# Performance work log

Measured on AMD Instinct MI355X. Metric: run time of the kernel, lower is better.

## Reference

```python
import jax, jax.numpy as jnp
import numpy as np

B, N, H, D = 16, 512, 8, 128  # batch, nodes, heads, hid_dim (per-head dim == hid_dim)


def setup_inputs() -> dict:
    key = jax.random.key(0)
    ks = jax.random.split(key, 12)
    x = jax.random.normal(ks[0], (B, N, D), dtype=jnp.float32)
    dist = jax.random.normal(ks[1], (B, N, N), dtype=jnp.float32)
    mask = (jax.random.uniform(ks[2], (B, N)) < 0.9).astype(jnp.float32)
    w_std = 0.02
    Wq = jax.random.normal(ks[3], (D, H * D), dtype=jnp.float32) * w_std
    Wk = jax.random.normal(ks[4], (D, H * D), dtype=jnp.float32) * w_std
    Wv = jax.random.normal(ks[5], (D, H * D), dtype=jnp.float32) * w_std
    Wo = jax.random.normal(ks[6], (H * D, D), dtype=jnp.float32) * w_std
    bq = jax.random.normal(ks[7], (H * D,), dtype=jnp.float32) * w_std
    bk = jax.random.normal(ks[8], (H * D,), dtype=jnp.float32) * w_std
    bv = jax.random.normal(ks[9], (H * D,), dtype=jnp.float32) * w_std
    bo = jax.random.normal(ks[10], (D,), dtype=jnp.float32) * w_std
    return {"x": x, "dist": dist, "mask": mask,
            "Wq": Wq, "bq": bq, "Wk": Wk, "bk": bk,
            "Wv": Wv, "bv": bv, "Wo": Wo, "bo": bo}


def reference(x, dist, mask, Wq, bq, Wk, bk, Wv, bv, Wo, bo):
    scale = jnp.asarray(D, x.dtype) ** -0.5
    # projections: [B,N,H*D] -> [B,H,N,D]
    q = (x @ Wq + bq).reshape(B, N, H, D).transpose(0, 2, 1, 3)
    k = (x @ Wk + bk).reshape(B, N, H, D).transpose(0, 2, 1, 3)
    v = (x @ Wv + bv).reshape(B, N, H, D).transpose(0, 2, 1, 3)
    m = mask[:, None, :, None]  # [B,1,N,1]
    q = q * m * scale
    k = k * m
    v = v * m
    a = jnp.einsum('bhnd,bhmd->bhnm', q, k)  # [B,H,N,N]
    a = a + dist[:, None, :, :]  # dist bias broadcast over heads
    amask = (mask[:, :, None] * mask[:, None, :])[:, None, :, :]  # [B,1,N,N]
    a = jnp.where(amask == 0, jnp.asarray(-1e9, a.dtype), a)
    a = jax.nn.softmax(a, axis=-1)
    a = jnp.where(amask == 0, jnp.asarray(0.0, a.dtype), a)
    y = jnp.einsum('bhnm,bhmd->bhnd', a, v)
    y = y.transpose(0, 2, 1, 3).reshape(B, N, H * D)
    y = y @ Wo + bo
    return y * mask[:, :, None]
```

## Files before the change

### kernel.cpp

```cpp
#include <hip/hip_runtime.h>
#include <hip/hip_bf16.h>

#define B_ 16
#define N_ 512
#define H_ 8
#define D_ 128
#define HD_ 1024
#define SCALE_ 0.08838834764831845f

typedef __attribute__((ext_vector_type(8))) short bf16x8;
typedef __attribute__((ext_vector_type(4))) float f32x4;
typedef __attribute__((ext_vector_type(4))) _Float16 f16x4;

__device__ __forceinline__ unsigned short f2bf(float f) {
    union { __hip_bfloat16 h; unsigned short u; } cv;
    cv.h = __float2bfloat16(f);
    return cv.u;
}
__device__ __forceinline__ float bf2f(unsigned short u) {
    union { unsigned int i; float f; } cv;
    cv.i = ((unsigned int)u) << 16;
    return cv.f;
}
__device__ __forceinline__ unsigned short f2h(float f) {
    union { _Float16 h; unsigned short u; } cv;
    cv.h = (_Float16)f;
    return cv.u;
}

__global__ __launch_bounds__(256) void prep_kernel(
    const float* __restrict__ Wq, const float* __restrict__ Wk,
    const float* __restrict__ Wv, const float* __restrict__ Wo,
    unsigned short* __restrict__ wTh, unsigned short* __restrict__ woT)
{
    __shared__ float T[32][33];
    const int tile = blockIdx.x;
    const int t = threadIdx.x;
    if (tile < 384) {
        const int w = tile / 128;
        const int rem = tile % 128;
        const int kt = rem & 3;
        const int ct = rem >> 2;
        const float* W = (w == 0) ? Wq : (w == 1) ? Wk : Wv;
        const int k0 = kt * 32, c0 = ct * 32;
        #pragma unroll
        for (int u = 0; u < 4; u++) {
            int lin = t + 256 * u; int r = lin >> 5, c = lin & 31;
            T[r][c] = W[(size_t)(k0 + r) * 1024 + c0 + c];
        }
        __syncthreads();
        unsigned short* oh = wTh + (size_t)w * 131072;
        #pragma unroll
        for (int u = 0; u < 4; u++) {
            int lin = t + 256 * u; int c = lin >> 5, r = lin & 31;
            oh[(size_t)(c0 + c) * 128 + k0 + r] = f2bf(T[r][c]);
        }
    } else {
        const int rem = tile - 384;
        const int nt = rem & 3;
        const int kt = rem >> 2;
        const int k0 = kt * 32, n0 = nt * 32;
        #pragma unroll
        for (int u = 0; u < 4; u++) {
            int lin = t + 256 * u; int r = lin >> 5, c = lin & 31;
            T[r][c] = Wo[(size_t)(k0 + r) * 128 + n0 + c];
        }
        __syncthreads();
        #pragma unroll
        for (int u = 0; u < 4; u++) {
            int lin = t + 256 * u; int c = lin >> 5, r = lin & 31;
            woT[(size_t)(n0 + c) * 1024 + k0 + r] = f2bf(T[r][c]);
        }
    }
}

__global__ __launch_bounds__(256, 2) void qkv_kernel(
    const float* __restrict__ x, const float* __restrict__ mask,
    const unsigned short* __restrict__ wTh,
    const float* __restrict__ bq, const float* __restrict__ bk,
    const float* __restrict__ bv,
    unsigned short* __restrict__ q, unsigned short* __restrict__ k,
    unsigned short* __restrict__ vT)
{
    const int cb = blockIdx.x % 24;
    const int by = blockIdx.x / 24;
    const int row0 = by * 128, c0 = cb * 128;
    const int which = c0 >> 10, w0 = c0 & 1023;
    const float* bi = (which == 0) ? bq : (which == 1) ? bk : bv;

    __shared__ alignas(16) unsigned short Wh[128][136];
    __shared__ float biS[128];
    __shared__ float mskS[128];

    const int t = threadIdx.x;
    if (t < 128) { biS[t] = bi[w0 + t]; mskS[t] = mask[row0 + t]; }

    const unsigned short* whp = wTh + (size_t)which * 131072 + (size_t)w0 * 128;
    #pragma unroll
    for (int u = 0; u < 8; u++) {
        int lin = t + 256 * u; int c = lin >> 4, k8 = (lin & 15) * 8;
        *(bf16x8*)&Wh[c][k8] = *(const bf16x8*)&whp[(size_t)c * 128 + k8];
    }

    const int wave = t >> 6, lane = t & 63, m16 = lane & 15, g4 = lane >> 4;
    const int rw = row0 + wave * 32;

    bf16x8 ah[2][4], al[2][4];
    #pragma unroll
    for (int mt = 0; mt < 2; mt++)
        #pragma unroll
        for (int kc = 0; kc < 4; kc++) {
            const float* xp = &x[(size_t)(rw + mt * 16 + m16) * 128 + kc * 32 + g4 * 8];
            float4 v0 = *(const float4*)xp;
            float4 v1 = *(const float4*)(xp + 4);
            float vv[8] = {v0.x, v0.y, v0.z, v0.w, v1.x, v1.y, v1.z, v1.w};
            union { bf16x8 v; unsigned short s[8]; } Hh, Ll;
            #pragma unroll
            for (int e = 0; e < 8; e++) {
                Hh.s[e] = f2bf(vv[e]);
                Ll.s[e] = f2bf(vv[e] - bf2f(Hh.s[e]));
            }
            ah[mt][kc] = Hh.v;
            al[mt][kc] = Ll.v;
        }
    __syncthreads();

    const f32x4 zero = {0.f, 0.f, 0.f, 0.f};
    f32x4 acc[2][8];
    #pragma unroll
    for (int mt = 0; mt < 2; mt++)
        #pragma unroll
        for (int nt = 0; nt < 8; nt++) acc[mt][nt] = zero;

    #pragma unroll
    for (int nt = 0; nt < 8; nt++) {
        #pragma unroll
        for (int kc = 0; kc < 4; kc++) {
            bf16x8 bh = *(const bf16x8*)&Wh[nt * 16 + m16][kc * 32 + g4 * 8];
            #pragma unroll
            for (int mt = 0; mt < 2; mt++) {
                acc[mt][nt] = __builtin_amdgcn_mfma_f32_16x16x32_bf16(ah[mt][kc], bh, acc[mt][nt], 0, 0, 0);
                acc[mt][nt] = __builtin_amdgcn_mfma_f32_16x16x32_bf16(al[mt][kc], bh, acc[mt][nt], 0, 0, 0);
            }
        }
    }
    __syncthreads();

    const int b = row0 >> 9, h = w0 >> 7;
    const int iseq0 = row0 & 511;
    unsigned short* Tr = &Wh[0][0];

    if (which == 2) {
        #pragma unroll
        for (int mt = 0; mt < 2; mt++)
            #pragma unroll
            for (int nt = 0; nt < 8; nt++)
                #pragma unroll
                for (int r = 0; r < 4; r++) {
                    int rowl = wave * 32 + mt * 16 + g4 * 4 + r;
                    int col = nt * 16 + m16;
                    Tr[col * 136 + rowl] = f2h((acc[mt][nt][r] + biS[col]) * mskS[rowl]);
                }
        __syncthreads();
        unsigned short* vbase = vT + (size_t)(b * 8 + h) * 128 * 512 + iseq0;
        #pragma unroll
        for (int u = 0; u < 8; u++) {
            int lin = t + 256 * u; int dl = lin >> 4, i8 = (lin & 15) * 8;
            *(bf16x8*)&vbase[(size_t)dl * 512 + i8] = *(const bf16x8*)&Tr[dl * 136 + i8];
        }
    } else {
        const float sc = (which == 0) ? SCALE_ : 1.0f;
        #pragma unroll
        for (int mt = 0; mt < 2; mt++)
            #pragma unroll
            for (int nt = 0; nt < 8; nt++)
                #pragma unroll
                for (int r = 0; r < 4; r++) {
                    int rowl = wave * 32 + mt * 16 + g4 * 4 + r;
                    int col = nt * 16 + m16;
                    Tr[rowl * 136 + col] = f2bf((acc[mt][nt][r] + biS[col]) * (mskS[rowl] * sc));
                }
        __syncthreads();
        unsigned short* dst = ((which == 0) ? q : k) +
                              ((size_t)(b * 8 + h) * 512 + iseq0) * 128;
        #pragma unroll
        for (int u = 0; u < 8; u++) {
            int lin = t + 256 * u; int rl = lin >> 4, c8 = (lin & 15) * 8;
            *(bf16x8*)&dst[(size_t)rl * 128 + c8] = *(const bf16x8*)&Tr[rl * 136 + c8];
        }
    }
}

__global__ __launch_bounds__(256, 2) void attn_kernel(
    const unsigned short* __restrict__ q, const unsigned short* __restrict__ k,
    const unsigned short* __restrict__ vT, const float* __restrict__ dist,
    const float* __restrict__ mask, unsigned short* __restrict__ y)
{
    const int xid = blockIdx.x;
    const int bh = (xid & 7) | ((xid >> 6) << 3);
    const int itile = (xid >> 3) & 7;
    const int b = bh >> 3, h = bh & 7;
    const int i0 = itile * 64;

    const unsigned short* qb = q + (size_t)bh * 512 * 128;
    const unsigned short* kb = k + (size_t)bh * 512 * 128;
    const unsigned short* vb = vT + (size_t)bh * 128 * 512;

    __shared__ alignas(16) unsigned short Ks[64][136];
    __shared__ alignas(16) unsigned short Vs[128][76];
    __shared__ alignas(16) float cmS[512];

    const int t = threadIdx.x;
    const int wave = t >> 6, lane = t & 63;
    const int m16 = lane & 15, g4 = lane >> 4;
    const int iw = i0 + wave * 16;

    cmS[t] = (mask[b * 512 + t] == 0.0f) ? -1e9f : 0.0f;
    cmS[256 + t] = (mask[b * 512 + 256 + t] == 0.0f) ? -1e9f : 0.0f;

    bf16x8 aq[4];
    #pragma unroll
    for (int c = 0; c < 4; c++)
        aq[c] = *(const bf16x8*)(qb + (size_t)(iw + m16) * 128 + c * 32 + g4 * 8);

    const int krow = t >> 2, kcol = (t & 3) * 32;
    const int vrow = t >> 1, vcol = (t & 1) * 32;

    const float* dbase = dist + ((size_t)b * 512 + iw) * 512;

    float4 dvA[4];
    {
        bf16x8 kp[4], vp[4];
        #pragma unroll
        for (int u = 0; u < 4; u++) {
            kp[u] = *(const bf16x8*)(kb + (size_t)krow * 128 + kcol + u * 8);
            vp[u] = *(const bf16x8*)(vb + (size_t)vrow * 512 + vcol + u * 8);
        }
        #pragma unroll
        for (int jt = 0; jt < 4; jt++)
            dvA[jt] = *(const float4*)&dbase[(size_t)m16 * 512 + jt * 16 + g4 * 4];
        #pragma unroll
        for (int u = 0; u < 4; u++) {
            *(bf16x8*)&Ks[krow][kcol + u * 8] = kp[u];
            union { bf16x8 v8; ushort4 h4[2]; } cv; cv.v8 = vp[u];
            *(ushort4*)&Vs[vrow][vcol + u * 8] = cv.h4[0];
            *(ushort4*)&Vs[vrow][vcol + u * 8 + 4] = cv.h4[1];
        }
    }
    __syncthreads();

    const f32x4 zero = {0.f, 0.f, 0.f, 0.f};
    float rm = -3.0e38f, rl = 0.f;
    f32x4 Ot[8] = {zero, zero, zero, zero, zero, zero, zero, zero};

    for (int c = 0; c < 8; c++) {
        const int j0 = c * 64;
        bf16x8 kp[4], vp[4];
        float4 dvB[4];
        if (c < 7) {
            const int j0n = j0 + 64;
            #pragma unroll
            for (int u = 0; u < 4; u++) {
                kp[u] = *(const bf16x8*)(kb + (size_t)(j0n + krow) * 128 + kcol + u * 8);
                vp[u] = *(const bf16x8*)(vb + (size_t)vrow * 512 + j0n + vcol + u * 8);
            }
            #pragma unroll
            for (int jt = 0; jt < 4; jt++)
                dvB[jt] = *(const float4*)&dbase[(size_t)m16 * 512 + j0n + jt * 16 + g4 * 4];
        }

        f32x4 s[4];
        #pragma unroll
        for (int jt = 0; jt < 4; jt++) {
            float4 cm4 = *(const float4*)&cmS[j0 + jt * 16 + g4 * 4];
            f32x4 a = {dvA[jt].x + cm4.x, dvA[jt].y + cm4.y,
                       dvA[jt].z + cm4.z, dvA[jt].w + cm4.w};
            #pragma unroll
            for (int cc = 0; cc < 4; cc++) {
                bf16x8 kf = *(const bf16x8*)&Ks[jt * 16 + m16][cc * 32 + g4 * 8];
                a = __builtin_amdgcn_mfma_f32_16x16x32_bf16(kf, aq[cc], a, 0, 0, 0);
            }
            s[jt] = a;
        }

        float cm = -3.0e38f;
        #pragma unroll
        for (int jt = 0; jt < 4; jt++)
            #pragma unroll
            for (int r = 0; r < 4; r++) cm = fmaxf(cm, s[jt][r]);
        cm = fmaxf(cm, __shfl_xor(cm, 16));
        cm = fmaxf(cm, __shfl_xor(cm, 32));

        float nm = fmaxf(rm, cm);
        float alpha = __expf(rm - nm);
        rm = nm;
        rl *= alpha;

        f16x4 pa[4];
        float ps = 0.f;
        #pragma unroll
        for (int jt = 0; jt < 4; jt++) {
            #pragma unroll
            for (int r = 0; r < 4; r++) {
                float p = __expf(s[jt][r] - rm);
                ps += p;
                pa[jt][r] = (_Float16)p;
            }
        }
        ps += __shfl_xor(ps, 16);
        ps += __shfl_xor(ps, 32);
        rl += ps;

        float a4[4];
        #pragma unroll
        for (int r = 0; r < 4; r++) a4[r] = __shfl(alpha, g4 * 4 + r);
        #pragma unroll
        for (int dt = 0; dt < 8; dt++)
            #pragma unroll
            for (int r = 0; r < 4; r++) Ot[dt][r] *= a4[r];

        #pragma unroll
        for (int jt = 0; jt < 4; jt++)
            #pragma unroll
            for (int dt = 0; dt < 8; dt++) {
                f16x4 vf = *(const f16x4*)&Vs[dt * 16 + m16][jt * 16 + g4 * 4];
                Ot[dt] = __builtin_amdgcn_mfma_f32_16x16x16f16(pa[jt], vf, Ot[dt], 0, 0, 0);
            }

        if (c < 7) {
            __syncthreads();
            #pragma unroll
            for (int u = 0; u < 4; u++) {
                *(bf16x8*)&Ks[krow][kcol + u * 8] = kp[u];
                union { bf16x8 v8; ushort4 h4[2]; } cv; cv.v8 = vp[u];
                *(ushort4*)&Vs[vrow][vcol + u * 8] = cv.h4[0];
                *(ushort4*)&Vs[vrow][vcol + u * 8 + 4] = cv.h4[1];
            }
            #pragma unroll
            for (int jt = 0; jt < 4; jt++) dvA[jt] = dvB[jt];
            __syncthreads();
        }
    }

    __syncthreads();
    float rs = (rl > 0.f) ? 1.0f / rl : 0.f;
    float rs4[4];
    #pragma unroll
    for (int r = 0; r < 4; r++) rs4[r] = __shfl(rs, g4 * 4 + r);
    #pragma unroll
    for (int dt = 0; dt < 8; dt++)
        #pragma unroll
        for (int r = 0; r < 4; r++)
            Ks[wave * 16 + g4 * 4 + r][dt * 16 + m16] = f2bf(Ot[dt][r] * rs4[r]);
    #pragma unroll
    for (int u = 0; u < 4; u++) {
        int lin = lane + 64 * u;
        int row = lin >> 4, seg = lin & 15;
        *(bf16x8*)&y[((size_t)(b * 512) + iw + row) * 1024 + h * 128 + seg * 8] =
            *(const bf16x8*)&Ks[wave * 16 + row][seg * 8];
    }
}

__global__ __launch_bounds__(256) void oproj_kernel(
    const unsigned short* __restrict__ Y, const unsigned short* __restrict__ woT,
    const float* __restrict__ bo, const float* __restrict__ mask,
    float* __restrict__ out)
{
    const int row0 = blockIdx.x * 32;
    __shared__ alignas(16) unsigned short Ys[32][136];
    __shared__ alignas(16) unsigned short Ws[128][136];
    __shared__ float boS[128];
    __shared__ float mskS[32];

    const int t = threadIdx.x;
    if (t < 128) boS[t] = bo[t];
    if (t < 32) mskS[t] = mask[row0 + t];

    const int wave = t >> 6, lane = t & 63;
    const int m16 = lane & 15, g4 = lane >> 4;
    const int mrow = (wave & 1) * 16, n0 = (wave >> 1) * 64;

    const int yr = t >> 4, yk = (t & 15) * 8;
    const int wn = t >> 4, wk = (t & 15) * 8;

    const f32x4 zero = {0.f, 0.f, 0.f, 0.f};
    f32x4 acc[4] = {zero, zero, zero, zero};

    bf16x8 yp[2], wp[8];
    #pragma unroll
    for (int u = 0; u < 2; u++)
        yp[u] = *(const bf16x8*)&Y[(size_t)(row0 + yr + u * 16) * 1024 + yk];
    #pragma unroll
    for (int u = 0; u < 8; u++)
        wp[u] = *(const bf16x8*)&woT[(size_t)(wn + u * 16) * 1024 + wk];

    for (int c = 0; c < 8; c++) {
        __syncthreads();
        #pragma unroll
        for (int u = 0; u < 2; u++) *(bf16x8*)&Ys[yr + u * 16][yk] = yp[u];
        #pragma unroll
        for (int u = 0; u < 8; u++) *(bf16x8*)&Ws[wn + u * 16][wk] = wp[u];
        __syncthreads();
        if (c < 7) {
            const int kc0 = (c + 1) * 128;
            #pragma unroll
            for (int u = 0; u < 2; u++)
                yp[u] = *(const bf16x8*)&Y[(size_t)(row0 + yr + u * 16) * 1024 + kc0 + yk];
            #pragma unroll
            for (int u = 0; u < 8; u++)
                wp[u] = *(const bf16x8*)&woT[(size_t)(wn + u * 16) * 1024 + kc0 + wk];
        }
        #pragma unroll
        for (int kc = 0; kc < 4; kc++) {
            bf16x8 a = *(const bf16x8*)&Ys[mrow + m16][kc * 32 + g4 * 8];
            #pragma unroll
            for (int nt = 0; nt < 4; nt++) {
                bf16x8 bb = *(const bf16x8*)&Ws[n0 + nt * 16 + m16][kc * 32 + g4 * 8];
                acc[nt] = __builtin_amdgcn_mfma_f32_16x16x32_bf16(a, bb, acc[nt], 0, 0, 0);
            }
        }
    }
    __syncthreads();

    float* Ot = (float*)&Ws[0][0];
    #pragma unroll
    for (int nt = 0; nt < 4; nt++)
        #pragma unroll
        for (int r = 0; r < 4; r++) {
            int rowl = mrow + g4 * 4 + r;
            int col = n0 + nt * 16 + m16;
            Ot[rowl * 132 + col] = (acc[nt][r] + boS[col]) * mskS[rowl];
        }
    __syncthreads();
    #pragma unroll
    for (int u = 0; u < 4; u++) {
        int lin = t + 256 * u; int r = lin >> 5, c4 = lin & 31;
        *(float4*)&out[(size_t)(row0 + r) * 128 + c4 * 4] =
            *(const float4*)&Ot[r * 132 + c4 * 4];
    }
}

extern "C" void kernel_launch(void* const* d_in, const int* in_sizes, int n_in,
                              void* d_out, int out_size, void* d_ws, size_t ws_size,
                              hipStream_t stream) {
    const float* x    = (const float*)d_in[0];
    const float* dist = (const float*)d_in[1];
    const float* mask = (const float*)d_in[2];
    const float* Wq   = (const float*)d_in[3];
    const float* bq   = (const float*)d_in[4];
    const float* Wk   = (const float*)d_in[5];
    const float* bk   = (const float*)d_in[6];
    const float* Wv   = (const float*)d_in[7];
    const float* bv   = (const float*)d_in[8];
    const float* Wo   = (const float*)d_in[9];
    const float* bo   = (const float*)d_in[10];
    float* out = (float*)d_out;

    const size_t per = (size_t)B_ * H_ * N_ * D_;
    unsigned short* qb  = (unsigned short*)d_ws;
    unsigned short* kb  = qb + per;
    unsigned short* vb  = kb + per;
    unsigned short* yb  = vb + per;
    unsigned short* wTh = yb + per;
    unsigned short* woT = wTh + 3 * 131072;

    prep_kernel<<<512, 256, 0, stream>>>(Wq, Wk, Wv, Wo, wTh, woT);
    qkv_kernel<<<1536, 256, 0, stream>>>(x, mask, wTh, bq, bk, bv, qb, kb, vb);
    attn_kernel<<<1024, 256, 0, stream>>>(qb, kb, vb, dist, mask, yb);
    oproj_kernel<<<256, 256, 0, stream>>>(yb, woT, bo, mask, out);
}
```

Baseline: 160.5 us.

## Read K/V fragments directly from global memory instead of LDS staging

Drops the shared-memory staging of K and V tiles, along with the register prefetch double-buffer and the per-chunk block barriers, in the attention kernel. Each wave now loads its MFMA fragments for K, V, dist and mask straight from global memory, relying on L1/L2 caching for reuse across the four waves. The min-2-blocks launch bound is removed since LDS use shrinks. This cuts barriers and LDS traffic, but the loads are narrower and uncoalesced, and global-load latency is no longer hidden by prefetching.

```diff
diff --git a/kernel.cpp b/kernel.cpp
--- a/kernel.cpp
+++ b/kernel.cpp
@@ -191,7 +191,7 @@
     }
 }
 
-__global__ __launch_bounds__(256, 2) void attn_kernel(
+__global__ __launch_bounds__(256) void attn_kernel(
     const unsigned short* __restrict__ q, const unsigned short* __restrict__ k,
     const unsigned short* __restrict__ vT, const float* __restrict__ dist,
     const float* __restrict__ mask, unsigned short* __restrict__ y)
@@ -206,78 +206,42 @@
     const unsigned short* kb = k + (size_t)bh * 512 * 128;
     const unsigned short* vb = vT + (size_t)bh * 128 * 512;
 
-    __shared__ alignas(16) unsigned short Ks[64][136];
-    __shared__ alignas(16) unsigned short Vs[128][76];
-    __shared__ alignas(16) float cmS[512];
+    __shared__ alignas(16) unsigned short Yst[64][136];
 
     const int t = threadIdx.x;
     const int wave = t >> 6, lane = t & 63;
     const int m16 = lane & 15, g4 = lane >> 4;
     const int iw = i0 + wave * 16;
 
-    cmS[t] = (mask[b * 512 + t] == 0.0f) ? -1e9f : 0.0f;
-    cmS[256 + t] = (mask[b * 512 + 256 + t] == 0.0f) ? -1e9f : 0.0f;
-
     bf16x8 aq[4];
     #pragma unroll
     for (int c = 0; c < 4; c++)
         aq[c] = *(const bf16x8*)(qb + (size_t)(iw + m16) * 128 + c * 32 + g4 * 8);
 
-    const int krow = t >> 2, kcol = (t & 3) * 32;
-    const int vrow = t >> 1, vcol = (t & 1) * 32;
-
     const float* dbase = dist + ((size_t)b * 512 + iw) * 512;
-
-    float4 dvA[4];
-    {
-        bf16x8 kp[4], vp[4];
-        #pragma unroll
-        for (int u = 0; u < 4; u++) {
-            kp[u] = *(const bf16x8*)(kb + (size_t)krow * 128 + kcol + u * 8);
-            vp[u] = *(const bf16x8*)(vb + (size_t)vrow * 512 + vcol + u * 8);
-        }
-        #pragma unroll
-        for (int jt = 0; jt < 4; jt++)
-            dvA[jt] = *(const float4*)&dbase[(size_t)m16 * 512 + jt * 16 + g4 * 4];
-        #pragma unroll
-        for (int u = 0; u < 4; u++) {
-            *(bf16x8*)&Ks[krow][kcol + u * 8] = kp[u];
-            union { bf16x8 v8; ushort4 h4[2]; } cv; cv.v8 = vp[u];
-            *(ushort4*)&Vs[vrow][vcol + u * 8] = cv.h4[0];
-            *(ushort4*)&Vs[vrow][vcol + u * 8 + 4] = cv.h4[1];
-        }
-    }
-    __syncthreads();
-
+    const float* mbase = mask + b * 512;
     const f32x4 zero = {0.f, 0.f, 0.f, 0.f};
+
     float rm = -3.0e38f, rl = 0.f;
     f32x4 Ot[8] = {zero, zero, zero, zero, zero, zero, zero, zero};
 
     for (int c = 0; c < 8; c++) {
         const int j0 = c * 64;
-        bf16x8 kp[4], vp[4];
-        float4 dvB[4];
-        if (c < 7) {
-            const int j0n = j0 + 64;
-            #pragma unroll
-            for (int u = 0; u < 4; u++) {
-                kp[u] = *(const bf16x8*)(kb + (size_t)(j0n + krow) * 128 + kcol + u * 8);
-                vp[u] = *(const bf16x8*)(vb + (size_t)vrow * 512 + j0n + vcol + u * 8);
-            }
-            #pragma unroll
-            for (int jt = 0; jt < 4; jt++)
-                dvB[jt] = *(const float4*)&dbase[(size_t)m16 * 512 + j0n + jt * 16 + g4 * 4];
-        }
 
         f32x4 s[4];
         #pragma unroll
         for (int jt = 0; jt < 4; jt++) {
-            float4 cm4 = *(const float4*)&cmS[j0 + jt * 16 + g4 * 4];
-            f32x4 a = {dvA[jt].x + cm4.x, dvA[jt].y + cm4.y,
-                       dvA[jt].z + cm4.z, dvA[jt].w + cm4.w};
+            const int jc = j0 + jt * 16 + g4 * 4;
+            float4 dv = *(const float4*)&dbase[(size_t)m16 * 512 + jc];
+            float4 mj = *(const float4*)&mbase[jc];
+            f32x4 a;
+            a[0] = (mj.x == 0.0f) ? -1e9f : dv.x;
+            a[1] = (mj.y == 0.0f) ? -1e9f : dv.y;
+            a[2] = (mj.z == 0.0f) ? -1e9f : dv.z;
+            a[3] = (mj.w == 0.0f) ? -1e9f : dv.w;
             #pragma unroll
             for (int cc = 0; cc < 4; cc++) {
-                bf16x8 kf = *(const bf16x8*)&Ks[jt * 16 + m16][cc * 32 + g4 * 8];
+                bf16x8 kf = *(const bf16x8*)(kb + (size_t)(j0 + jt * 16 + m16) * 128 + cc * 32 + g4 * 8);
                 a = __builtin_amdgcn_mfma_f32_16x16x32_bf16(kf, aq[cc], a, 0, 0, 0);
             }
             s[jt] = a;
@@ -320,29 +284,15 @@
             for (int r = 0; r < 4; r++) Ot[dt][r] *= a4[r];
 
         #pragma unroll
-        for (int jt = 0; jt < 4; jt++)
-            #pragma unroll
-            for (int dt = 0; dt < 8; dt++) {
-                f16x4 vf = *(const f16x4*)&Vs[dt * 16 + m16][jt * 16 + g4 * 4];
+        for (int dt = 0; dt < 8; dt++) {
+            #pragma unroll
+            for (int jt = 0; jt < 4; jt++) {
+                f16x4 vf = *(const f16x4*)(vb + (size_t)(dt * 16 + m16) * 512 + j0 + jt * 16 + g4 * 4);
                 Ot[dt] = __builtin_amdgcn_mfma_f32_16x16x16f16(pa[jt], vf, Ot[dt], 0, 0, 0);
             }
-
-        if (c < 7) {
-            __syncthreads();
-            #pragma unroll
-            for (int u = 0; u < 4; u++) {
-                *(bf16x8*)&Ks[krow][kcol + u * 8] = kp[u];
-                union { bf16x8 v8; ushort4 h4[2]; } cv; cv.v8 = vp[u];
-                *(ushort4*)&Vs[vrow][vcol + u * 8] = cv.h4[0];
-                *(ushort4*)&Vs[vrow][vcol + u * 8 + 4] = cv.h4[1];
-            }
-            #pragma unroll
-            for (int jt = 0; jt < 4; jt++) dvA[jt] = dvB[jt];
-            __syncthreads();
-        }
-    }
-
-    __syncthreads();
+        }
+    }
+
     float rs = (rl > 0.f) ? 1.0f / rl : 0.f;
     float rs4[4];
     #pragma unroll
@@ -351,13 +301,13 @@
     for (int dt = 0; dt < 8; dt++)
         #pragma unroll
         for (int r = 0; r < 4; r++)
-            Ks[wave * 16 + g4 * 4 + r][dt * 16 + m16] = f2bf(Ot[dt][r] * rs4[r]);
+            Yst[wave * 16 + g4 * 4 + r][dt * 16 + m16] = f2bf(Ot[dt][r] * rs4[r]);
     #pragma unroll
     for (int u = 0; u < 4; u++) {
         int lin = lane + 64 * u;
         int row = lin >> 4, seg = lin & 15;
         *(bf16x8*)&y[((size_t)(b * 512) + iw + row) * 1024 + h * 128 + seg * 8] =
-            *(const bf16x8*)&Ks[wave * 16 + row][seg * 8];
+            *(const bf16x8*)&Yst[wave * 16 + row][seg * 8];
     }
 }
 
```

New measurement: 306.1 us. 90.7% more time.
